# Kernel optimization log

Hardware: AMD Instinct MI355X
Metric: run time of the kernel (lower is better)

The kernel has to match this reference:

```python
import jax, jax.numpy as jnp
import numpy as np

B, L, D = 2, 2048, 1024
H, K = 16, 16
HD = D // H


def setup_inputs() -> dict:
    key = jax.random.key(0)
    k1, k2, k3, k4, k5 = jax.random.split(key, 5)
    x = jax.random.normal(k1, (B, L, D), dtype=jnp.float32)
    # Linear weight (out_features, in_features), small init to keep logits sane
    w_in = jax.random.normal(k2, (3 * D, D), dtype=jnp.float32) * 0.02
    # TISA radial-basis kernel parameters, per (head, kernel)
    kernel_offsets = jax.random.normal(k3, (H, K), dtype=jnp.float32) * 20.0
    kernel_amplitudes = 0.1 + 0.01 * jax.random.normal(k4, (H, K), dtype=jnp.float32)
    kernel_sharpness = 0.1 + 0.01 * jax.random.normal(k5, (H, K), dtype=jnp.float32)
    return {"x": x, "w_in": w_in, "kernel_offsets": kernel_offsets,
            "kernel_amplitudes": kernel_amplitudes, "kernel_sharpness": kernel_sharpness}


def tisa_bias(offsets, amplitudes, sharpness, seq_len):
    # relative positions -(L-1) .. (L-1)  -> per-head RBF positional scores
    rel = jnp.arange(-(seq_len - 1), seq_len, dtype=jnp.float32)  # (2L-1,)
    # scores[h, m] = sum_k amp[h,k] * exp(-|sharp[h,k]| * (off[h,k] - rel[m])^2)
    diff = offsets[:, :, None] - rel[None, None, :]               # (H, K, 2L-1)
    scores = jnp.sum(amplitudes[:, :, None] * jnp.exp(-jnp.abs(sharpness)[:, :, None] * diff * diff), axis=1)  # (H, 2L-1)
    # Toeplitz expansion: bias[h, i, j] = scores[h, (i - j) + (L-1)]
    i = jnp.arange(seq_len)
    idx = i[:, None] - i[None, :] + (seq_len - 1)                 # (L, L)
    return scores[:, idx]                                         # (H, L, L)


def reference(x, w_in, kernel_offsets, kernel_amplitudes, kernel_sharpness):
    b, l, d = x.shape
    proj = jnp.einsum('bld,ed->ble', x, w_in)                     # (B, L, 3D)
    # split: memory = first 2D (k then v), query = last D
    k_, v_, q_ = proj[..., :d], proj[..., d:2 * d], proj[..., 2 * d:]

    def heads(t):
        return t.reshape(b, l, H, HD).transpose(0, 2, 1, 3)       # (B, H, L, HD)

    q, k, v = heads(q_), heads(k_), heads(v_)
    bias = tisa_bias(kernel_offsets, kernel_amplitudes, kernel_sharpness, l)  # (H, L, L)
    scale = 1.0 / np.sqrt(HD).astype(np.float32)
    logits = jnp.einsum('bhld,bhmd->bhlm', q, k) * scale + bias[None]
    attn = jax.nn.softmax(logits, axis=-1)
    out = jnp.einsum('bhlm,bhmd->bhld', attn, v)                  # (B, H, L, HD)
    return out.transpose(0, 2, 1, 3).reshape(b, l, d)             # (B, L, D)
```

## Files before the change

kernel.cpp:

```cpp
#include <hip/hip_runtime.h>
#include <hip/hip_bf16.h>
#include <stdint.h>
#include <stddef.h>


#define NB     2
#define NH     16
#define SL     2048
#define DH     64
#define DMODEL 1024
#define SCP    4096

typedef __attribute__((ext_vector_type(8)))  short bf16x8;
typedef __attribute__((ext_vector_type(4)))  short bf16x4;
typedef __attribute__((ext_vector_type(4)))  float f32x4;
typedef __attribute__((ext_vector_type(16))) float f32x16;

static __device__ __forceinline__ short f2bf(float x) {
  __hip_bfloat16 h = __float2bfloat16(x);
  return *reinterpret_cast<short*>(&h);
}
static __device__ __forceinline__ long long bf4_to_ll(bf16x4 v) {
  long long r; __builtin_memcpy(&r, &v, 8); return r;
}
static __device__ __forceinline__ bf16x4 ll_to_bf4(long long v) {
  bf16x4 r; __builtin_memcpy(&r, &v, 8); return r;
}
#define GLD(g, l) __builtin_amdgcn_global_load_lds( \
    (const __attribute__((address_space(1))) void*)(g), \
    (__attribute__((address_space(3))) void*)(l), 16, 0, 0)

__global__ __launch_bounds__(256) void cvt_bf16_k(const float* __restrict__ src,
                                                  short* __restrict__ dst, int n4) {
  int i = blockIdx.x * 256 + threadIdx.x;
  if (i >= n4) return;
  float4 a = *(const float4*)(src + (size_t)i * 4);
  bf16x4 o;
  o.x = f2bf(a.x); o.y = f2bf(a.y); o.z = f2bf(a.z); o.w = f2bf(a.w);
  *(bf16x4*)(dst + (size_t)i * 4) = o;
}

__global__ void tisa_bias_k(const float* __restrict__ koff,
                            const float* __restrict__ kamp,
                            const float* __restrict__ kshp,
                            float* __restrict__ scores) {
  int h = blockIdx.y;
  int r = blockIdx.x * 256 + threadIdx.x;
  if (r >= 4095) return;
  float rel = (float)(r - (SL - 1));
  float acc = 0.f;
#pragma unroll
  for (int k = 0; k < 16; ++k) {
    float o = koff[h * 16 + k];
    float a = kamp[h * 16 + k];
    float s = fabsf(kshp[h * 16 + k]);
    float d = o - rel;
    acc += a * __expf(-s * d * d);
  }
  scores[h * SCP + r] = acc;
}

__global__ __launch_bounds__(256) void qkv_gemm_k(
    const short* __restrict__ A, const short* __restrict__ Bw,
    __hip_bfloat16* __restrict__ kbuf, __hip_bfloat16* __restrict__ vbufT,
    __hip_bfloat16* __restrict__ qbuf) {
  __shared__ __align__(16) short As[128 * 64];
  __shared__ __align__(16) short Bs[128 * 64];
  const int tid  = threadIdx.x;
  const int lane = tid & 63;
  const int wv   = tid >> 6;
  const int l15  = lane & 15, quad = lane >> 4;
  const int wm = (wv & 1) * 64, wn = (wv >> 1) * 64;
  const int m0 = blockIdx.y * 128, n0 = blockIdx.x * 128;

  f32x4 acc[4][4];
#pragma unroll
  for (int r = 0; r < 4; ++r)
#pragma unroll
    for (int c = 0; c < 4; ++c) acc[r][c] = (f32x4){0.f, 0.f, 0.f, 0.f};

  for (int kt = 0; kt < 16; ++kt) {
    const int k0 = kt * 64;
#pragma unroll
    for (int it = 0; it < 4; ++it) {
      const int e8  = it * 256 + tid;
      const int row = e8 >> 3;
      const int col = (e8 & 7) * 8;
      GLD(A + (size_t)(m0 + row) * DMODEL + k0 + col, &As[e8 * 8]);
      GLD(Bw + (size_t)(n0 + row) * DMODEL + k0 + col, &Bs[e8 * 8]);
    }
    __syncthreads();
#pragma unroll
    for (int ki = 0; ki < 64; ki += 32) {
      bf16x8 af[4], bfv[4];
#pragma unroll
      for (int r = 0; r < 4; ++r)
        af[r] = *(const bf16x8*)&As[(wm + r * 16 + l15) * 64 + ki + quad * 8];
#pragma unroll
      for (int c = 0; c < 4; ++c)
        bfv[c] = *(const bf16x8*)&Bs[(wn + c * 16 + l15) * 64 + ki + quad * 8];
#pragma unroll
      for (int r = 0; r < 4; ++r)
#pragma unroll
        for (int c = 0; c < 4; ++c)
          acc[r][c] = __builtin_amdgcn_mfma_f32_16x16x32_bf16(af[r], bfv[c], acc[r][c], 0, 0, 0);
    }
    __syncthreads();
  }
#pragma unroll
  for (int c = 0; c < 4; ++c) {
    const int n     = n0 + wn + c * 16 + l15;
    const int which = n >> 10;
    const int hh    = (n >> 6) & 15;
    const int hd    = n & 63;
#pragma unroll
    for (int r = 0; r < 4; ++r) {
      const int m0r = m0 + wm + r * 16 + quad * 4;
      const int bb  = m0r >> 11;
      const int ll  = m0r & 2047;
      if (which == 1) {
        bf16x4 pk;
#pragma unroll
        for (int g = 0; g < 4; ++g) pk[g] = f2bf(acc[r][c][g]);
        *(bf16x4*)&vbufT[(((size_t)bb * NH + hh) * DH + hd) * SL + ll] = pk;
      } else if (which == 0) {
#pragma unroll
        for (int g = 0; g < 4; ++g)
          kbuf[(((size_t)bb * NH + hh) * SL + ll + g) * DH + hd] = __float2bfloat16(acc[r][c][g]);
      } else {
#pragma unroll
        for (int g = 0; g < 4; ++g)
          qbuf[(((size_t)bb * NH + hh) * SL + ll + g) * DH + hd] = __float2bfloat16(acc[r][c][g] * 0.125f);
      }
    }
  }
}

__global__ __launch_bounds__(128, 2) void attn_k(
    const __hip_bfloat16* __restrict__ qbuf, const __hip_bfloat16* __restrict__ kbuf,
    const __hip_bfloat16* __restrict__ vbufT, const float* __restrict__ scores,
    float* __restrict__ out) {
  __shared__ __align__(16) short Ks[64 * 72];
  __shared__ __align__(16) short Vs[64 * 72];
  __shared__ __align__(16) float Bss[2112];
  const int bh   = blockIdx.x;
  const int b    = bh >> 4, h = bh & 15;
  const int tid  = threadIdx.x;
  const int lane = tid & 63;
  const int wv   = tid >> 6;
  const int n32  = lane & 31, hf = lane >> 5;
  const int i0b  = blockIdx.y * 64;
  const int i0   = i0b + wv * 32;
  const __hip_bfloat16* qb = qbuf + (size_t)bh * SL * DH;
  const short* kb = (const short*)(kbuf + (size_t)bh * SL * DH);
  const short* vb = (const short*)(vbufT + (size_t)bh * DH * SL);
  const float* sc = scores + h * SCP;

  {
    const float* bsrc = sc + i0b;
#pragma unroll
    for (int i = 0; i < 4; ++i)
      GLD(bsrc + (size_t)(i * 128 + tid) * 4, &Bss[(i * 128 + tid) * 4]);
    if (tid < 16) GLD(bsrc + (size_t)(512 + tid) * 4, &Bss[(512 + tid) * 4]);
  }

  bf16x8 qf[4];
#pragma unroll
  for (int kc = 0; kc < 4; ++kc)
    qf[kc] = *(const bf16x8*)&qb[(size_t)(i0 + n32) * DH + kc * 16 + hf * 8];

  f32x16 ot[2];
#pragma unroll
  for (int dt = 0; dt < 2; ++dt)
#pragma unroll
    for (int r = 0; r < 16; ++r) ot[dt][r] = 0.f;
  float lsum = 0.f;

  for (int j0 = 0; j0 < SL; j0 += 64) {
    {
      const short* ksrc = kb + (size_t)j0 * DH;
#pragma unroll
      for (int i = 0; i < 4; ++i) {
        int c = i * 128 + tid; int r = c / 9, s = c - r * 9;
        GLD(ksrc + (size_t)r * DH + s * 8, &Ks[c * 8]);
      }
      if (tid < 64) {
        int c = 512 + tid; int r = c / 9, s = c - r * 9;
        GLD(ksrc + (size_t)r * DH + s * 8, &Ks[c * 8]);
      }
    }
    {
#pragma unroll
      for (int i = 0; i < 4; ++i) {
        int c = i * 128 + tid; int r = c / 9, s = c - r * 9;
        GLD(vb + (size_t)r * SL + j0 + s * 8, &Vs[c * 8]);
      }
      if (tid < 64) {
        int c = 512 + tid; int r = c / 9, s = c - r * 9;
        GLD(vb + (size_t)r * SL + j0 + s * 8, &Vs[c * 8]);
      }
    }
    __syncthreads();

#pragma unroll
    for (int kt = 0; kt < 2; ++kt) {
      f32x16 st;
#pragma unroll
      for (int r = 0; r < 16; ++r) st[r] = 0.f;
#pragma unroll
      for (int kc = 0; kc < 4; ++kc) {
        bf16x8 kf = *(const bf16x8*)&Ks[(kt * 32 + n32) * 72 + kc * 16 + hf * 8];
        st = __builtin_amdgcn_mfma_f32_32x32x16_bf16(kf, qf[kc], st, 0, 0, 0);
      }
      bf16x4 pk[4];
      const int tb0 = wv * 32 + n32 - j0 - kt * 32 - 4 * hf + 2047;
#pragma unroll
      for (int g = 0; g < 4; ++g) {
        const int tb = tb0 - 8 * g;
#pragma unroll
        for (int i = 0; i < 4; ++i) {
          const float p = __expf(st[g * 4 + i] + Bss[tb - i]);
          lsum += p;
          pk[g][i] = f2bf(p);
        }
      }
      long long s0 = hf ? bf4_to_ll(pk[0]) : bf4_to_ll(pk[1]);
      bf16x4 r0 = ll_to_bf4(__shfl_xor(s0, 32));
      bf16x8 pf0 = hf == 0 ? __builtin_shufflevector(pk[0], r0, 0, 1, 2, 3, 4, 5, 6, 7)
                           : __builtin_shufflevector(r0, pk[1], 0, 1, 2, 3, 4, 5, 6, 7);
      long long s1 = hf ? bf4_to_ll(pk[2]) : bf4_to_ll(pk[3]);
      bf16x4 r1 = ll_to_bf4(__shfl_xor(s1, 32));
      bf16x8 pf1 = hf == 0 ? __builtin_shufflevector(pk[2], r1, 0, 1, 2, 3, 4, 5, 6, 7)
                           : __builtin_shufflevector(r1, pk[3], 0, 1, 2, 3, 4, 5, 6, 7);
#pragma unroll
      for (int dt = 0; dt < 2; ++dt) {
        const short* vr = &Vs[(dt * 32 + n32) * 72 + kt * 32];
        bf16x8 vf0 = *(const bf16x8*)&vr[hf * 8];
        bf16x8 vf1 = *(const bf16x8*)&vr[16 + hf * 8];
        ot[dt] = __builtin_amdgcn_mfma_f32_32x32x16_bf16(vf0, pf0, ot[dt], 0, 0, 0);
        ot[dt] = __builtin_amdgcn_mfma_f32_32x32x16_bf16(vf1, pf1, ot[dt], 0, 0, 0);
      }
    }
    __syncthreads();
  }

  lsum += __shfl_xor(lsum, 32);
  const float inv = 1.f / lsum;
  float* orow = out + (((size_t)b * SL + i0 + n32) * NH + h) * DH;
#pragma unroll
  for (int dt = 0; dt < 2; ++dt)
#pragma unroll
    for (int g = 0; g < 4; ++g) {
      f32x4 v;
#pragma unroll
      for (int i = 0; i < 4; ++i) v[i] = ot[dt][g * 4 + i] * inv;
      *(f32x4*)&orow[dt * 32 + 8 * g + 4 * hf] = v;
    }
}

extern "C" void kernel_launch(void* const* d_in, const int* in_sizes, int n_in,
                              void* d_out, int out_size, void* d_ws, size_t ws_size,
                              hipStream_t stream) {
  const float* x    = (const float*)d_in[0];
  const float* w    = (const float*)d_in[1];
  const float* koff = (const float*)d_in[2];
  const float* kamp = (const float*)d_in[3];
  const float* kshp = (const float*)d_in[4];
  float* out = (float*)d_out;

  const size_t per = (size_t)NB * NH * SL * DH;
  const size_t nx  = (size_t)NB * SL * DMODEL;
  const size_t nw  = (size_t)3 * DMODEL * DMODEL;

  __hip_bfloat16* kbuf  = (__hip_bfloat16*)d_ws;
  __hip_bfloat16* vbufT = kbuf + per;
  __hip_bfloat16* qbuf  = vbufT + per;
  float* scores = (float*)(qbuf + per);
  short* xbf    = (short*)(scores + (size_t)NH * SCP);
  short* wbf    = xbf + nx;

  cvt_bf16_k<<<(int)(nx / 4 + 255) / 256, 256, 0, stream>>>(x, xbf, (int)(nx / 4));
  cvt_bf16_k<<<(int)(nw / 4 + 255) / 256, 256, 0, stream>>>(w, wbf, (int)(nw / 4));
  tisa_bias_k<<<dim3(16, NH), 256, 0, stream>>>(koff, kamp, kshp, scores);
  qkv_gemm_k<<<dim3(24, 32), 256, 0, stream>>>(xbf, wbf, kbuf, vbufT, qbuf);
  attn_k<<<dim3(NB * NH, SL / 64), 128, 0, stream>>>(qbuf, kbuf, vbufT, scores, out);
}
```

Before: 202.6 us.

## Fuse prep kernels and stage QKV GEMM epilogue through LDS for coalesced stores

Merges the two bf16 conversion kernels and the TISA bias kernel into one launch, which removes two kernel launches and their serialization gaps. The QKV GEMM epilogue now writes accumulators into a padded shared-memory tile, then issues 16-byte coalesced global stores for K/Q (row-major) and for transposed V. Before, those stores were scattered 2-byte and 8-byte writes. The change costs an extra barrier and LDS round trip in the epilogue, and the shared buffer grows to hold the padded output tile.

```diff
diff --git a/kernel.cpp b/kernel.cpp
--- a/kernel.cpp
+++ b/kernel.cpp
@@ -10,6 +10,7 @@
 #define DH     64
 #define DMODEL 1024
 #define SCP    4096
+#define CTS    136
 
 typedef __attribute__((ext_vector_type(8)))  short bf16x8;
 typedef __attribute__((ext_vector_type(4)))  short bf16x4;
@@ -30,48 +31,54 @@
     (const __attribute__((address_space(1))) void*)(g), \
     (__attribute__((address_space(3))) void*)(l), 16, 0, 0)
 
-__global__ __launch_bounds__(256) void cvt_bf16_k(const float* __restrict__ src,
-                                                  short* __restrict__ dst, int n4) {
-  int i = blockIdx.x * 256 + threadIdx.x;
-  if (i >= n4) return;
-  float4 a = *(const float4*)(src + (size_t)i * 4);
-  bf16x4 o;
-  o.x = f2bf(a.x); o.y = f2bf(a.y); o.z = f2bf(a.z); o.w = f2bf(a.w);
-  *(bf16x4*)(dst + (size_t)i * 4) = o;
-}
-
-__global__ void tisa_bias_k(const float* __restrict__ koff,
-                            const float* __restrict__ kamp,
-                            const float* __restrict__ kshp,
-                            float* __restrict__ scores) {
-  int h = blockIdx.y;
-  int r = blockIdx.x * 256 + threadIdx.x;
-  if (r >= 4095) return;
-  float rel = (float)(r - (SL - 1));
-  float acc = 0.f;
-#pragma unroll
-  for (int k = 0; k < 16; ++k) {
-    float o = koff[h * 16 + k];
-    float a = kamp[h * 16 + k];
-    float s = fabsf(kshp[h * 16 + k]);
-    float d = o - rel;
-    acc += a * __expf(-s * d * d);
-  }
-  scores[h * SCP + r] = acc;
+__global__ __launch_bounds__(256) void prep_k(
+    const float* __restrict__ x, const float* __restrict__ w,
+    const float* __restrict__ koff, const float* __restrict__ kamp,
+    const float* __restrict__ kshp,
+    short* __restrict__ xbf, short* __restrict__ wbf,
+    float* __restrict__ scores) {
+  const int bx = blockIdx.x, tid = threadIdx.x;
+  if (bx < 7168) {
+    const float* src = (bx < 4096) ? x : w;
+    short* dst       = (bx < 4096) ? xbf : wbf;
+    const int i      = (bx < 4096 ? bx : bx - 4096) * 256 + tid;
+    float4 a = *(const float4*)(src + (size_t)i * 4);
+    bf16x4 o;
+    o.x = f2bf(a.x); o.y = f2bf(a.y); o.z = f2bf(a.z); o.w = f2bf(a.w);
+    *(bf16x4*)(dst + (size_t)i * 4) = o;
+  } else {
+    const int idx = bx - 7168;
+    const int h = idx >> 4;
+    const int r = (idx & 15) * 256 + tid;
+    if (r >= 4095) return;
+    float rel = (float)(r - (SL - 1));
+    float acc = 0.f;
+#pragma unroll
+    for (int k = 0; k < 16; ++k) {
+      float o = koff[h * 16 + k];
+      float a = kamp[h * 16 + k];
+      float s = fabsf(kshp[h * 16 + k]);
+      float d = o - rel;
+      acc += a * __expf(-s * d * d);
+    }
+    scores[h * SCP + r] = acc;
+  }
 }
 
 __global__ __launch_bounds__(256) void qkv_gemm_k(
     const short* __restrict__ A, const short* __restrict__ Bw,
     __hip_bfloat16* __restrict__ kbuf, __hip_bfloat16* __restrict__ vbufT,
     __hip_bfloat16* __restrict__ qbuf) {
-  __shared__ __align__(16) short As[128 * 64];
-  __shared__ __align__(16) short Bs[128 * 64];
+  __shared__ __align__(16) short SM[128 * CTS];
+  short* As = SM;
+  short* Bs = SM + 128 * 64;
   const int tid  = threadIdx.x;
   const int lane = tid & 63;
   const int wv   = tid >> 6;
   const int l15  = lane & 15, quad = lane >> 4;
   const int wm = (wv & 1) * 64, wn = (wv >> 1) * 64;
   const int m0 = blockIdx.y * 128, n0 = blockIdx.x * 128;
+  const int which = n0 >> 10;
 
   f32x4 acc[4][4];
 #pragma unroll
@@ -107,31 +114,50 @@
     }
     __syncthreads();
   }
-#pragma unroll
-  for (int c = 0; c < 4; ++c) {
-    const int n     = n0 + wn + c * 16 + l15;
-    const int which = n >> 10;
-    const int hh    = (n >> 6) & 15;
-    const int hd    = n & 63;
-#pragma unroll
-    for (int r = 0; r < 4; ++r) {
-      const int m0r = m0 + wm + r * 16 + quad * 4;
-      const int bb  = m0r >> 11;
-      const int ll  = m0r & 2047;
-      if (which == 1) {
+
+  const int bb  = m0 >> 11;
+  const int llb = m0 & 2047;
+  const int hhb = (n0 >> 6) & 15;
+  if (which != 1) {
+    const float qs = (which == 2) ? 0.125f : 1.0f;
+#pragma unroll
+    for (int r = 0; r < 4; ++r)
+#pragma unroll
+      for (int c = 0; c < 4; ++c)
+#pragma unroll
+        for (int g = 0; g < 4; ++g)
+          SM[(wm + r * 16 + quad * 4 + g) * CTS + wn + c * 16 + l15] =
+              f2bf(acc[r][c][g] * qs);
+    __syncthreads();
+    __hip_bfloat16* dst = (which == 0) ? kbuf : qbuf;
+#pragma unroll
+    for (int i = 0; i < 8; ++i) {
+      const int cidx = i * 256 + tid;
+      const int m = cidx >> 4, ch = cidx & 15;
+      bf16x8 val = *(const bf16x8*)&SM[m * CTS + ch * 8];
+      const int hh  = hhb + (ch >> 3);
+      const int hd0 = (ch & 7) * 8;
+      *(bf16x8*)&dst[(((size_t)bb * NH + hh) * SL + llb + m) * DH + hd0] = val;
+    }
+  } else {
+#pragma unroll
+    for (int r = 0; r < 4; ++r)
+#pragma unroll
+      for (int c = 0; c < 4; ++c) {
         bf16x4 pk;
 #pragma unroll
         for (int g = 0; g < 4; ++g) pk[g] = f2bf(acc[r][c][g]);
-        *(bf16x4*)&vbufT[(((size_t)bb * NH + hh) * DH + hd) * SL + ll] = pk;
-      } else if (which == 0) {
-#pragma unroll
-        for (int g = 0; g < 4; ++g)
-          kbuf[(((size_t)bb * NH + hh) * SL + ll + g) * DH + hd] = __float2bfloat16(acc[r][c][g]);
-      } else {
-#pragma unroll
-        for (int g = 0; g < 4; ++g)
-          qbuf[(((size_t)bb * NH + hh) * SL + ll + g) * DH + hd] = __float2bfloat16(acc[r][c][g] * 0.125f);
-      }
+        *(bf16x4*)&SM[(wn + c * 16 + l15) * CTS + wm + r * 16 + quad * 4] = pk;
+      }
+    __syncthreads();
+#pragma unroll
+    for (int i = 0; i < 8; ++i) {
+      const int cidx = i * 256 + tid;
+      const int n = cidx >> 4, ch = cidx & 15;
+      bf16x8 val = *(const bf16x8*)&SM[n * CTS + ch * 8];
+      const int hh = hhb + (n >> 6);
+      const int hd = n & 63;
+      *(bf16x8*)&vbufT[(((size_t)bb * NH + hh) * DH + hd) * SL + llb + ch * 8] = val;
     }
   }
 }
@@ -279,9 +305,7 @@
   short* xbf    = (short*)(scores + (size_t)NH * SCP);
   short* wbf    = xbf + nx;
 
-  cvt_bf16_k<<<(int)(nx / 4 + 255) / 256, 256, 0, stream>>>(x, xbf, (int)(nx / 4));
-  cvt_bf16_k<<<(int)(nw / 4 + 255) / 256, 256, 0, stream>>>(w, wbf, (int)(nw / 4));
-  tisa_bias_k<<<dim3(16, NH), 256, 0, stream>>>(koff, kamp, kshp, scores);
+  prep_k<<<7424, 256, 0, stream>>>(x, w, koff, kamp, kshp, xbf, wbf, scores);
   qkv_gemm_k<<<dim3(24, 32), 256, 0, stream>>>(xbf, wbf, kbuf, vbufT, qbuf);
   attn_k<<<dim3(NB * NH, SL / 64), 128, 0, stream>>>(qbuf, kbuf, vbufT, scores, out);
 }
```

Measured after the change: 197.3 us. 1.03x faster.
